# Kernel tuning notes

Measured on AMD Instinct MI355X. Metric: run time of the kernel, lower is better.

The kernel has to match this reference:

```python
import jax, jax.numpy as jnp
import numpy as np

D_MODEL = 1024
D_STATE = 16
DT_RANK = 64  # ceil(1024/16)
DT_MIN, DT_MAX = 1e-3, 1e-1


def setup_inputs() -> dict:
    key = jax.random.key(0)
    ks = jax.random.split(key, 6)
    x = jax.random.normal(ks[0], (2, 2048, D_MODEL), jnp.float32)
    A_log = jax.random.normal(ks[1], (D_MODEL, D_STATE), jnp.float32)
    D = jax.random.normal(ks[2], (D_MODEL,), jnp.float32)
    # nn.Linear default init ~ U(-1/sqrt(fan_in), 1/sqrt(fan_in)); normal*scale is fine for a baseline
    x_proj_w = jax.random.normal(ks[3], (DT_RANK + 2 * D_STATE, D_MODEL), jnp.float32) * (D_MODEL ** -0.5)
    dt_init_std = DT_RANK ** -0.5
    dt_proj_w = jax.random.uniform(ks[4], (D_MODEL, DT_RANK), jnp.float32, -dt_init_std, dt_init_std)
    dt = jnp.exp(jax.random.uniform(ks[5], (D_MODEL,), jnp.float32)
                 * (np.log(DT_MAX) - np.log(DT_MIN)) + np.log(DT_MIN))
    dt_proj_b = dt + jnp.log(-jnp.expm1(-dt))  # inverse-softplus init
    return {"x": x, "A_log": A_log, "D": D, "x_proj_w": x_proj_w,
            "dt_proj_w": dt_proj_w, "dt_proj_b": dt_proj_b}


def _s6(x, A_log, D, x_proj_w, dt_proj_w, dt_proj_b):
    A = -jnp.exp(A_log)                                    # (d, n)
    xp = jnp.einsum('bld,ed->ble', x, x_proj_w)            # (b, l, r+2n)
    d_rank = xp[..., :DT_RANK]
    Bm = xp[..., DT_RANK:DT_RANK + D_STATE]                # (b, l, n)
    Cm = xp[..., DT_RANK + D_STATE:]                       # (b, l, n)
    delta = jax.nn.softplus(jnp.einsum('blr,dr->bld', d_rank, dt_proj_w) + dt_proj_b)
    deltaA = jnp.exp(jnp.einsum('bld,dn->bldn', delta, A))          # (b, l, d, n)
    deltaB_u = jnp.einsum('bld,bln,bld->bldn', delta, Bm, x)        # (b, l, d, n)

    def step(h, inp):
        dA_t, dBu_t, C_t = inp          # (b,d,n), (b,d,n), (b,n)
        h = dA_t * h + dBu_t
        y = jnp.einsum('bdn,bn->bd', h, C_t)
        return h, y

    b, l, d = x.shape
    h0 = jnp.zeros((b, d, D_STATE), x.dtype)
    _, ys = jax.lax.scan(step, h0,
                         (deltaA.transpose(1, 0, 2, 3),
                          deltaB_u.transpose(1, 0, 2, 3),
                          Cm.transpose(1, 0, 2)))
    y = ys.transpose(1, 0, 2) + x * D                      # (b, l, d)
    return y


def reference(x, A_log, D, x_proj_w, dt_proj_w, dt_proj_b):
    return _s6(x, A_log, D, x_proj_w, dt_proj_w, dt_proj_b)
```

## Files before the change

### kernel.cpp

```cpp
#include <hip/hip_runtime.h>
#include <math.h>

#define Bb 2
#define Ll 2048
#define Dm 1024
#define Ns 16
#define Rr 64
#define Ee 96
#define XPS 8
#define BLK (Bb*Ll)
#define NTHR 256

__global__ void __launch_bounds__(NTHR)
k_xproj(const float* __restrict__ x, const float* __restrict__ xw,
        float* __restrict__ xp_part) {
    __shared__ float xs[64 * 37];
    __shared__ float wsh[96 * 37];
    int bx = blockIdx.x;
    int ks = bx & 7, mt = bx >> 3;
    int i0 = mt * 64;
    int tid = threadIdx.x;
    int tx = tid & 15, ty = tid >> 4;
    float acc[4][6];
#pragma unroll
    for (int ii = 0; ii < 4; ++ii)
#pragma unroll
        for (int jj = 0; jj < 6; ++jj) acc[ii][jj] = 0.f;

    for (int kc = 0; kc < 4; ++kc) {
        int k0 = ks * 128 + kc * 32;
        for (int t = tid; t < 512; t += NTHR) {
            int r = t >> 3, c = (t & 7) * 4;
            float4 v = *(const float4*)(x + (size_t)(i0 + r) * Dm + k0 + c);
            xs[r*37+c] = v.x; xs[r*37+c+1] = v.y; xs[r*37+c+2] = v.z; xs[r*37+c+3] = v.w;
        }
        for (int t = tid; t < 768; t += NTHR) {
            int r = t >> 3, c = (t & 7) * 4;
            float4 v = *(const float4*)(xw + (size_t)r * Dm + k0 + c);
            wsh[r*37+c] = v.x; wsh[r*37+c+1] = v.y; wsh[r*37+c+2] = v.z; wsh[r*37+c+3] = v.w;
        }
        __syncthreads();
#pragma unroll 8
        for (int k = 0; k < 32; ++k) {
            float xv[4], wv[6];
#pragma unroll
            for (int ii = 0; ii < 4; ++ii) xv[ii] = xs[(ty*4+ii)*37 + k];
#pragma unroll
            for (int jj = 0; jj < 6; ++jj) wv[jj] = wsh[(tx*6+jj)*37 + k];
#pragma unroll
            for (int ii = 0; ii < 4; ++ii)
#pragma unroll
                for (int jj = 0; jj < 6; ++jj)
                    acc[ii][jj] = fmaf(xv[ii], wv[jj], acc[ii][jj]);
        }
        __syncthreads();
    }
#pragma unroll
    for (int ii = 0; ii < 4; ++ii)
#pragma unroll
        for (int jj = 0; jj < 6; ++jj)
            xp_part[((size_t)ks * BLK + (i0 + ty*4 + ii)) * Ee + tx*6 + jj] = acc[ii][jj];
}

__global__ void __launch_bounds__(NTHR)
k_prep(const float* __restrict__ xp_part, float* __restrict__ xp) {
    int g = blockIdx.x * NTHR + threadIdx.x;
    const float4* p = (const float4*)xp_part;
    float4 s = p[g];
#pragma unroll
    for (int i = 1; i < XPS; ++i) {
        float4 v = p[(size_t)i * (BLK * Ee / 4) + g];
        s.x += v.x; s.y += v.y; s.z += v.z; s.w += v.w;
    }
    ((float4*)xp)[g] = s;
}

__global__ void __launch_bounds__(NTHR)
k_delta(const float* __restrict__ xp, const float* __restrict__ dtw,
        const float* __restrict__ dtb, float* __restrict__ delta) {
    __shared__ float xs[64 * 65];
    __shared__ float wsh[64 * 65];
    int bx = blockIdx.x;
    int nt = bx & 15, mt = bx >> 4;
    int i0 = mt * 64, j0 = nt * 64;
    int tid = threadIdx.x, tx = tid & 15, ty = tid >> 4;

    for (int t = tid; t < 1024; t += NTHR) {
        int r = t >> 4, c = (t & 15) * 4;
        float4 v = *(const float4*)(xp + (size_t)(i0 + r) * Ee + c);
        xs[r*65+c] = v.x; xs[r*65+c+1] = v.y; xs[r*65+c+2] = v.z; xs[r*65+c+3] = v.w;
        float4 w = *(const float4*)(dtw + (size_t)(j0 + r) * Rr + c);
        wsh[r*65+c] = w.x; wsh[r*65+c+1] = w.y; wsh[r*65+c+2] = w.z; wsh[r*65+c+3] = w.w;
    }
    __syncthreads();

    float acc[4][4];
#pragma unroll
    for (int ii = 0; ii < 4; ++ii)
#pragma unroll
        for (int jj = 0; jj < 4; ++jj) acc[ii][jj] = 0.f;
#pragma unroll 8
    for (int k = 0; k < 64; ++k) {
        float xv[4], wv[4];
#pragma unroll
        for (int ii = 0; ii < 4; ++ii) xv[ii] = xs[(ty*4+ii)*65 + k];
#pragma unroll
        for (int jj = 0; jj < 4; ++jj) wv[jj] = wsh[(tx*4+jj)*65 + k];
#pragma unroll
        for (int ii = 0; ii < 4; ++ii)
#pragma unroll
            for (int jj = 0; jj < 4; ++jj)
                acc[ii][jj] = fmaf(xv[ii], wv[jj], acc[ii][jj]);
    }
    int d0 = j0 + tx * 4;
    float4 bias = *(const float4*)(dtb + d0);
#pragma unroll
    for (int ii = 0; ii < 4; ++ii) {
        int bl = i0 + ty*4 + ii;
        float z0 = acc[ii][0] + bias.x, z1 = acc[ii][1] + bias.y;
        float z2 = acc[ii][2] + bias.z, z3 = acc[ii][3] + bias.w;
        float4 o;
        o.x = fmaxf(z0, 0.f) + log1pf(__expf(-fabsf(z0)));
        o.y = fmaxf(z1, 0.f) + log1pf(__expf(-fabsf(z1)));
        o.z = fmaxf(z2, 0.f) + log1pf(__expf(-fabsf(z2)));
        o.w = fmaxf(z3, 0.f) + log1pf(__expf(-fabsf(z3)));
        *(float4*)(delta + (size_t)bl * Dm + d0) = o;
    }
}

__device__ inline void load_a(const float* __restrict__ A_log, int d, float* a) {
    const float4* Ap = (const float4*)(A_log + (size_t)d * Ns);
    float4 a0 = Ap[0], a1 = Ap[1], a2 = Ap[2], a3 = Ap[3];
    float tmp[Ns] = {a0.x,a0.y,a0.z,a0.w, a1.x,a1.y,a1.z,a1.w,
                     a2.x,a2.y,a2.z,a2.w, a3.x,a3.y,a3.z,a3.w};
#pragma unroll
    for (int n = 0; n < Ns; ++n) a[n] = -__expf(tmp[n]);
}

template<int CHv>
__global__ void __launch_bounds__(NTHR)
k_scan_part(const float* __restrict__ delta, const float* __restrict__ x,
            const float* __restrict__ xp, const float* __restrict__ A_log,
            float* __restrict__ Ec, float* __restrict__ Sc) {
    constexpr int CLv = Ll / CHv;
    int bx = blockIdx.x;
    int dblk = bx & 3, chunk = (bx >> 2) & (CHv - 1), b = bx >> 2 >> __builtin_ctz(CHv);
    int tid = threadIdx.x;
    int d = dblk * 256 + tid;
    int row0 = b * Ll + chunk * CLv;

    float a[Ns], h[Ns];
    load_a(A_log, d, a);
#pragma unroll
    for (int n = 0; n < Ns; ++n) h[n] = 0.f;
    float sd = 0.f;

#pragma unroll 4
    for (int t = 0; t < CLv; ++t) {
        size_t row = (size_t)(row0 + t);
        float dl = delta[row * Dm + d];
        float xv = x[row * Dm + d];
        const float* bp = xp + row * Ee + Rr;
        float4 B0 = *(const float4*)(bp + 0),  B1 = *(const float4*)(bp + 4);
        float4 B2 = *(const float4*)(bp + 8),  B3 = *(const float4*)(bp + 12);
        float Bv[Ns] = {B0.x,B0.y,B0.z,B0.w, B1.x,B1.y,B1.z,B1.w,
                        B2.x,B2.y,B2.z,B2.w, B3.x,B3.y,B3.z,B3.w};
        float dx = dl * xv;
        sd += dl;
#pragma unroll
        for (int n = 0; n < Ns; ++n)
            h[n] = fmaf(__expf(dl * a[n]), h[n], dx * Bv[n]);
    }
    size_t base = ((size_t)b * CHv + chunk) * Dm + d;
    float4* Ep = (float4*)(Ec + base * Ns);
    Ep[0] = make_float4(h[0],  h[1],  h[2],  h[3]);
    Ep[1] = make_float4(h[4],  h[5],  h[6],  h[7]);
    Ep[2] = make_float4(h[8],  h[9],  h[10], h[11]);
    Ep[3] = make_float4(h[12], h[13], h[14], h[15]);
    Sc[base] = sd;
}

template<int CHv>
__global__ void __launch_bounds__(NTHR)
k_combine(const float* __restrict__ Ec, const float* __restrict__ Sc,
          const float* __restrict__ A_log, float* __restrict__ Hin) {
    int gid = blockIdx.x * NTHR + threadIdx.x;
    int n = gid & (Ns - 1);
    int d = (gid >> 4) & (Dm - 1);
    int b = gid >> 14;
    float a = -__expf(A_log[d * Ns + n]);
    float h = 0.f;
    for (int c = 0; c < CHv; ++c) {
        size_t base = ((size_t)b * CHv + c) * Dm + d;
        Hin[base * Ns + n] = h;
        float P = __expf(a * Sc[base]);
        h = fmaf(P, h, Ec[base * Ns + n]);
    }
}

template<int CHv>
__global__ void __launch_bounds__(NTHR)
k_scan_full(const float* __restrict__ delta, const float* __restrict__ x,
            const float* __restrict__ xp, const float* __restrict__ A_log,
            const float* __restrict__ Dp, const float* __restrict__ Hin,
            float* __restrict__ out) {
    constexpr int CLv = Ll / CHv;
    int bx = blockIdx.x;
    int dblk = bx & 3, chunk = (bx >> 2) & (CHv - 1), b = bx >> 2 >> __builtin_ctz(CHv);
    int tid = threadIdx.x;
    int d = dblk * 256 + tid;
    int row0 = b * Ll + chunk * CLv;

    float a[Ns], h[Ns];
    load_a(A_log, d, a);
    size_t base = ((size_t)b * CHv + chunk) * Dm + d;
    {
        const float4* Hp = (const float4*)(Hin + base * Ns);
        float4 h0 = Hp[0], h1 = Hp[1], h2 = Hp[2], h3 = Hp[3];
        h[0]=h0.x; h[1]=h0.y; h[2]=h0.z; h[3]=h0.w;
        h[4]=h1.x; h[5]=h1.y; h[6]=h1.z; h[7]=h1.w;
        h[8]=h2.x; h[9]=h2.y; h[10]=h2.z; h[11]=h2.w;
        h[12]=h3.x; h[13]=h3.y; h[14]=h3.z; h[15]=h3.w;
    }
    float Dval = Dp[d];

#pragma unroll 4
    for (int t = 0; t < CLv; ++t) {
        size_t row = (size_t)(row0 + t);
        float dl = delta[row * Dm + d];
        float xv = x[row * Dm + d];
        const float* bp = xp + row * Ee + Rr;
        float4 B0 = *(const float4*)(bp + 0),  B1 = *(const float4*)(bp + 4);
        float4 B2 = *(const float4*)(bp + 8),  B3 = *(const float4*)(bp + 12);
        float4 C0 = *(const float4*)(bp + 16), C1 = *(const float4*)(bp + 20);
        float4 C2 = *(const float4*)(bp + 24), C3 = *(const float4*)(bp + 28);
        float Bv[Ns] = {B0.x,B0.y,B0.z,B0.w, B1.x,B1.y,B1.z,B1.w,
                        B2.x,B2.y,B2.z,B2.w, B3.x,B3.y,B3.z,B3.w};
        float Cv[Ns] = {C0.x,C0.y,C0.z,C0.w, C1.x,C1.y,C1.z,C1.w,
                        C2.x,C2.y,C2.z,C2.w, C3.x,C3.y,C3.z,C3.w};
        float dx = dl * xv;
        float y = 0.f;
#pragma unroll
        for (int n = 0; n < Ns; ++n) {
            h[n] = fmaf(__expf(dl * a[n]), h[n], dx * Bv[n]);
            y = fmaf(h[n], Cv[n], y);
        }
        out[row * Dm + d] = fmaf(xv, Dval, y);
    }
}

extern "C" void kernel_launch(void* const* d_in, const int* in_sizes, int n_in,
                              void* d_out, int out_size, void* d_ws, size_t ws_size,
                              hipStream_t stream) {
    const float* x     = (const float*)d_in[0];
    const float* A_log = (const float*)d_in[1];
    const float* Dp    = (const float*)d_in[2];
    const float* xw    = (const float*)d_in[3];
    const float* dtw   = (const float*)d_in[4];
    const float* dtb   = (const float*)d_in[5];
    float* out = (float*)d_out;
    float* ws  = (float*)d_ws;

    float* xp      = ws;
    float* delta   = xp + 393216;
    float* S3      = delta + 4194304;
    float* xp_part = S3;

    k_xproj<<<dim3(512),  dim3(NTHR), 0, stream>>>(x, xw, xp_part);
    k_prep <<<dim3(384),  dim3(NTHR), 0, stream>>>(xp_part, xp);
    k_delta<<<dim3(1024), dim3(NTHR), 0, stream>>>(xp, dtw, dtb, delta);

    size_t need128 = (size_t)(393216 + 4194304 + 8650752) * 4;
    if (ws_size >= need128) {
        constexpr int CHv = 128;
        float* Ec  = S3;
        float* Sc  = Ec + (size_t)Bb*CHv*Dm*Ns;
        float* Hin = Sc + (size_t)Bb*CHv*Dm;
        k_scan_part<CHv><<<dim3(Bb*CHv*4), dim3(NTHR), 0, stream>>>(delta, x, xp, A_log, Ec, Sc);
        k_combine  <CHv><<<dim3(128),      dim3(NTHR), 0, stream>>>(Ec, Sc, A_log, Hin);
        k_scan_full<CHv><<<dim3(Bb*CHv*4), dim3(NTHR), 0, stream>>>(delta, x, xp, A_log, Dp, Hin, out);
    } else {
        constexpr int CHv = 64;
        float* Ec  = S3;
        float* Sc  = Ec + (size_t)Bb*CHv*Dm*Ns;
        float* Hin = Sc + (size_t)Bb*CHv*Dm;
        k_scan_part<CHv><<<dim3(Bb*CHv*4), dim3(NTHR), 0, stream>>>(delta, x, xp, A_log, Ec, Sc);
        k_combine  <CHv><<<dim3(128),      dim3(NTHR), 0, stream>>>(Ec, Sc, A_log, Hin);
        k_scan_full<CHv><<<dim3(Bb*CHv*4), dim3(NTHR), 0, stream>>>(delta, x, xp, A_log, Dp, Hin, out);
    }
}
```

Measured before the change: 165.4 us.

## Fuse split-K reduction, delta projection and chunk scan into one kernel

Merges the split-K partial-sum reduction, the dt projection with softplus, and the first-pass chunk scan into a single kernel. Delta and B values for each 64-row tile stay in shared memory and feed the local scan without a round trip through global memory. The chunk count is fixed at 64 chunks of 32 steps. The x-projection tile grows to 128 rows, with transposed shared layouts that allow vector LDS reads. Only 256 blocks run the fused kernel and each uses large shared memory, so occupancy and parallelism in the scan phase drop.

```diff
diff --git a/kernel.cpp b/kernel.cpp
--- a/kernel.cpp
+++ b/kernel.cpp
@@ -10,45 +10,51 @@
 #define XPS 8
 #define BLK (Bb*Ll)
 #define NTHR 256
+#define CH 64
+#define CL 32
 
 __global__ void __launch_bounds__(NTHR)
 k_xproj(const float* __restrict__ x, const float* __restrict__ xw,
         float* __restrict__ xp_part) {
-    __shared__ float xs[64 * 37];
-    __shared__ float wsh[96 * 37];
+    __shared__ float xsT[32 * 132];
+    __shared__ float wT [32 * 100];
     int bx = blockIdx.x;
     int ks = bx & 7, mt = bx >> 3;
-    int i0 = mt * 64;
+    int i0 = mt * 128;
     int tid = threadIdx.x;
     int tx = tid & 15, ty = tid >> 4;
-    float acc[4][6];
-#pragma unroll
-    for (int ii = 0; ii < 4; ++ii)
+
+    float acc[8][6];
+#pragma unroll
+    for (int ii = 0; ii < 8; ++ii)
 #pragma unroll
         for (int jj = 0; jj < 6; ++jj) acc[ii][jj] = 0.f;
 
     for (int kc = 0; kc < 4; ++kc) {
         int k0 = ks * 128 + kc * 32;
-        for (int t = tid; t < 512; t += NTHR) {
+        for (int t = tid; t < 1024; t += NTHR) {
             int r = t >> 3, c = (t & 7) * 4;
             float4 v = *(const float4*)(x + (size_t)(i0 + r) * Dm + k0 + c);
-            xs[r*37+c] = v.x; xs[r*37+c+1] = v.y; xs[r*37+c+2] = v.z; xs[r*37+c+3] = v.w;
+            xsT[(c+0)*132 + r] = v.x; xsT[(c+1)*132 + r] = v.y;
+            xsT[(c+2)*132 + r] = v.z; xsT[(c+3)*132 + r] = v.w;
         }
         for (int t = tid; t < 768; t += NTHR) {
             int r = t >> 3, c = (t & 7) * 4;
             float4 v = *(const float4*)(xw + (size_t)r * Dm + k0 + c);
-            wsh[r*37+c] = v.x; wsh[r*37+c+1] = v.y; wsh[r*37+c+2] = v.z; wsh[r*37+c+3] = v.w;
+            wT[(c+0)*100 + r] = v.x; wT[(c+1)*100 + r] = v.y;
+            wT[(c+2)*100 + r] = v.z; wT[(c+3)*100 + r] = v.w;
         }
         __syncthreads();
 #pragma unroll 8
         for (int k = 0; k < 32; ++k) {
-            float xv[4], wv[6];
-#pragma unroll
-            for (int ii = 0; ii < 4; ++ii) xv[ii] = xs[(ty*4+ii)*37 + k];
-#pragma unroll
-            for (int jj = 0; jj < 6; ++jj) wv[jj] = wsh[(tx*6+jj)*37 + k];
-#pragma unroll
-            for (int ii = 0; ii < 4; ++ii)
+            float xv[8], wv[6];
+            *(float4*)(xv)   = *(const float4*)(xsT + k*132 + ty*8);
+            *(float4*)(xv+4) = *(const float4*)(xsT + k*132 + ty*8 + 4);
+            *(float2*)(wv)   = *(const float2*)(wT + k*100 + tx*6);
+            *(float2*)(wv+2) = *(const float2*)(wT + k*100 + tx*6 + 2);
+            *(float2*)(wv+4) = *(const float2*)(wT + k*100 + tx*6 + 4);
+#pragma unroll
+            for (int ii = 0; ii < 8; ++ii)
 #pragma unroll
                 for (int jj = 0; jj < 6; ++jj)
                     acc[ii][jj] = fmaf(xv[ii], wv[jj], acc[ii][jj]);
@@ -56,131 +62,139 @@
         __syncthreads();
     }
 #pragma unroll
-    for (int ii = 0; ii < 4; ++ii)
+    for (int ii = 0; ii < 8; ++ii)
 #pragma unroll
         for (int jj = 0; jj < 6; ++jj)
-            xp_part[((size_t)ks * BLK + (i0 + ty*4 + ii)) * Ee + tx*6 + jj] = acc[ii][jj];
-}
-
-__global__ void __launch_bounds__(NTHR)
-k_prep(const float* __restrict__ xp_part, float* __restrict__ xp) {
-    int g = blockIdx.x * NTHR + threadIdx.x;
-    const float4* p = (const float4*)xp_part;
-    float4 s = p[g];
-#pragma unroll
-    for (int i = 1; i < XPS; ++i) {
-        float4 v = p[(size_t)i * (BLK * Ee / 4) + g];
-        s.x += v.x; s.y += v.y; s.z += v.z; s.w += v.w;
-    }
-    ((float4*)xp)[g] = s;
-}
-
-__global__ void __launch_bounds__(NTHR)
-k_delta(const float* __restrict__ xp, const float* __restrict__ dtw,
-        const float* __restrict__ dtb, float* __restrict__ delta) {
-    __shared__ float xs[64 * 65];
-    __shared__ float wsh[64 * 65];
+            xp_part[((size_t)ks * BLK + (i0 + ty*8 + ii)) * Ee + tx*6 + jj] = acc[ii][jj];
+}
+
+__global__ void __launch_bounds__(NTHR)
+k_dscan(const float* __restrict__ xp_part, const float* __restrict__ dtw,
+        const float* __restrict__ dtb, const float* __restrict__ x,
+        const float* __restrict__ A_log,
+        float* __restrict__ delta, float* __restrict__ xpBC,
+        float* __restrict__ Ec, float* __restrict__ Sc) {
+    __shared__ float xsT[64 * 68];
+    __shared__ float wdT[64 * 260];
+    __shared__ float BCs[64 * 33];
     int bx = blockIdx.x;
-    int nt = bx & 15, mt = bx >> 4;
-    int i0 = mt * 64, j0 = nt * 64;
-    int tid = threadIdx.x, tx = tid & 15, ty = tid >> 4;
+    int nt = bx & 3, mt = bx >> 2;
+    int i0 = mt * 64, j0 = nt * 256;
+    int tid = threadIdx.x;
+    int tx = tid & 15, ty = tid >> 4;
 
     for (int t = tid; t < 1024; t += NTHR) {
         int r = t >> 4, c = (t & 15) * 4;
-        float4 v = *(const float4*)(xp + (size_t)(i0 + r) * Ee + c);
-        xs[r*65+c] = v.x; xs[r*65+c+1] = v.y; xs[r*65+c+2] = v.z; xs[r*65+c+3] = v.w;
-        float4 w = *(const float4*)(dtw + (size_t)(j0 + r) * Rr + c);
-        wsh[r*65+c] = w.x; wsh[r*65+c+1] = w.y; wsh[r*65+c+2] = w.z; wsh[r*65+c+3] = w.w;
+        float4 s = make_float4(0.f, 0.f, 0.f, 0.f);
+#pragma unroll
+        for (int sI = 0; sI < XPS; ++sI) {
+            float4 v = *(const float4*)(xp_part + ((size_t)sI * BLK + i0 + r) * Ee + c);
+            s.x += v.x; s.y += v.y; s.z += v.z; s.w += v.w;
+        }
+        xsT[(c+0)*68 + r] = s.x; xsT[(c+1)*68 + r] = s.y;
+        xsT[(c+2)*68 + r] = s.z; xsT[(c+3)*68 + r] = s.w;
+    }
+    for (int t = tid; t < 512; t += NTHR) {
+        int r = t >> 3, cc = (t & 7) * 4;
+        float4 s = make_float4(0.f, 0.f, 0.f, 0.f);
+#pragma unroll
+        for (int sI = 0; sI < XPS; ++sI) {
+            float4 v = *(const float4*)(xp_part + ((size_t)sI * BLK + i0 + r) * Ee + Rr + cc);
+            s.x += v.x; s.y += v.y; s.z += v.z; s.w += v.w;
+        }
+        BCs[r*33 + cc+0] = s.x; BCs[r*33 + cc+1] = s.y;
+        BCs[r*33 + cc+2] = s.z; BCs[r*33 + cc+3] = s.w;
+        if (nt == 0) *(float4*)(xpBC + (size_t)(i0 + r) * 32 + cc) = s;
+    }
+    for (int t = tid; t < 4096; t += NTHR) {
+        int r = t >> 4, c = (t & 15) * 4;
+        float4 v = *(const float4*)(dtw + (size_t)(j0 + r) * Rr + c);
+        wdT[(c+0)*260 + r] = v.x; wdT[(c+1)*260 + r] = v.y;
+        wdT[(c+2)*260 + r] = v.z; wdT[(c+3)*260 + r] = v.w;
     }
     __syncthreads();
 
-    float acc[4][4];
+    float acc[4][16];
 #pragma unroll
     for (int ii = 0; ii < 4; ++ii)
 #pragma unroll
-        for (int jj = 0; jj < 4; ++jj) acc[ii][jj] = 0.f;
-#pragma unroll 8
+        for (int jj = 0; jj < 16; ++jj) acc[ii][jj] = 0.f;
+#pragma unroll 4
     for (int k = 0; k < 64; ++k) {
-        float xv[4], wv[4];
-#pragma unroll
-        for (int ii = 0; ii < 4; ++ii) xv[ii] = xs[(ty*4+ii)*65 + k];
-#pragma unroll
-        for (int jj = 0; jj < 4; ++jj) wv[jj] = wsh[(tx*4+jj)*65 + k];
+        float xv[4], wv[16];
+        *(float4*)xv = *(const float4*)(xsT + k*68 + ty*4);
+#pragma unroll
+        for (int g = 0; g < 4; ++g)
+            *(float4*)(wv + 4*g) = *(const float4*)(wdT + k*260 + g*64 + tx*4);
 #pragma unroll
         for (int ii = 0; ii < 4; ++ii)
 #pragma unroll
-            for (int jj = 0; jj < 4; ++jj)
+            for (int jj = 0; jj < 16; ++jj)
                 acc[ii][jj] = fmaf(xv[ii], wv[jj], acc[ii][jj]);
     }
-    int d0 = j0 + tx * 4;
-    float4 bias = *(const float4*)(dtb + d0);
-#pragma unroll
-    for (int ii = 0; ii < 4; ++ii) {
-        int bl = i0 + ty*4 + ii;
-        float z0 = acc[ii][0] + bias.x, z1 = acc[ii][1] + bias.y;
-        float z2 = acc[ii][2] + bias.z, z3 = acc[ii][3] + bias.w;
-        float4 o;
-        o.x = fmaxf(z0, 0.f) + log1pf(__expf(-fabsf(z0)));
-        o.y = fmaxf(z1, 0.f) + log1pf(__expf(-fabsf(z1)));
-        o.z = fmaxf(z2, 0.f) + log1pf(__expf(-fabsf(z2)));
-        o.w = fmaxf(z3, 0.f) + log1pf(__expf(-fabsf(z3)));
-        *(float4*)(delta + (size_t)bl * Dm + d0) = o;
-    }
-}
-
-__device__ inline void load_a(const float* __restrict__ A_log, int d, float* a) {
-    const float4* Ap = (const float4*)(A_log + (size_t)d * Ns);
-    float4 a0 = Ap[0], a1 = Ap[1], a2 = Ap[2], a3 = Ap[3];
-    float tmp[Ns] = {a0.x,a0.y,a0.z,a0.w, a1.x,a1.y,a1.z,a1.w,
-                     a2.x,a2.y,a2.z,a2.w, a3.x,a3.y,a3.z,a3.w};
-#pragma unroll
-    for (int n = 0; n < Ns; ++n) a[n] = -__expf(tmp[n]);
-}
-
-template<int CHv>
-__global__ void __launch_bounds__(NTHR)
-k_scan_part(const float* __restrict__ delta, const float* __restrict__ x,
-            const float* __restrict__ xp, const float* __restrict__ A_log,
-            float* __restrict__ Ec, float* __restrict__ Sc) {
-    constexpr int CLv = Ll / CHv;
-    int bx = blockIdx.x;
-    int dblk = bx & 3, chunk = (bx >> 2) & (CHv - 1), b = bx >> 2 >> __builtin_ctz(CHv);
-    int tid = threadIdx.x;
-    int d = dblk * 256 + tid;
-    int row0 = b * Ll + chunk * CLv;
-
-    float a[Ns], h[Ns];
-    load_a(A_log, d, a);
-#pragma unroll
-    for (int n = 0; n < Ns; ++n) h[n] = 0.f;
-    float sd = 0.f;
-
+    __syncthreads();
+
+    float* deltaT = wdT;
+#pragma unroll
+    for (int g = 0; g < 4; ++g) {
+        int dl0 = g*64 + tx*4;
+        float4 bias = *(const float4*)(dtb + j0 + dl0);
+#pragma unroll
+        for (int ii = 0; ii < 4; ++ii) {
+            int tloc = ty*4 + ii;
+            float z0 = acc[ii][g*4+0] + bias.x, z1 = acc[ii][g*4+1] + bias.y;
+            float z2 = acc[ii][g*4+2] + bias.z, z3 = acc[ii][g*4+3] + bias.w;
+            float4 o;
+            o.x = fmaxf(z0, 0.f) + log1pf(__expf(-fabsf(z0)));
+            o.y = fmaxf(z1, 0.f) + log1pf(__expf(-fabsf(z1)));
+            o.z = fmaxf(z2, 0.f) + log1pf(__expf(-fabsf(z2)));
+            o.w = fmaxf(z3, 0.f) + log1pf(__expf(-fabsf(z3)));
+            *(float4*)(deltaT + tloc*260 + dl0) = o;
+            *(float4*)(delta + (size_t)(i0 + tloc) * Dm + j0 + dl0) = o;
+        }
+    }
+    __syncthreads();
+
+    int dloc = tid, d = j0 + dloc;
+    float a[Ns];
+    {
+        const float4* Ap = (const float4*)(A_log + (size_t)d * Ns);
+        float4 a0 = Ap[0], a1 = Ap[1], a2 = Ap[2], a3 = Ap[3];
+        float tmp[Ns] = {a0.x,a0.y,a0.z,a0.w, a1.x,a1.y,a1.z,a1.w,
+                         a2.x,a2.y,a2.z,a2.w, a3.x,a3.y,a3.z,a3.w};
+#pragma unroll
+        for (int n = 0; n < Ns; ++n) a[n] = -__expf(tmp[n]);
+    }
+#pragma unroll
+    for (int ch = 0; ch < 2; ++ch) {
+        int row0 = i0 + ch * CL;
+        int b = row0 >> 11, c = (row0 & (Ll - 1)) >> 5;
+        float h[Ns];
+#pragma unroll
+        for (int n = 0; n < Ns; ++n) h[n] = 0.f;
+        float sd = 0.f;
 #pragma unroll 4
-    for (int t = 0; t < CLv; ++t) {
-        size_t row = (size_t)(row0 + t);
-        float dl = delta[row * Dm + d];
-        float xv = x[row * Dm + d];
-        const float* bp = xp + row * Ee + Rr;
-        float4 B0 = *(const float4*)(bp + 0),  B1 = *(const float4*)(bp + 4);
-        float4 B2 = *(const float4*)(bp + 8),  B3 = *(const float4*)(bp + 12);
-        float Bv[Ns] = {B0.x,B0.y,B0.z,B0.w, B1.x,B1.y,B1.z,B1.w,
-                        B2.x,B2.y,B2.z,B2.w, B3.x,B3.y,B3.z,B3.w};
-        float dx = dl * xv;
-        sd += dl;
-#pragma unroll
-        for (int n = 0; n < Ns; ++n)
-            h[n] = fmaf(__expf(dl * a[n]), h[n], dx * Bv[n]);
-    }
-    size_t base = ((size_t)b * CHv + chunk) * Dm + d;
-    float4* Ep = (float4*)(Ec + base * Ns);
-    Ep[0] = make_float4(h[0],  h[1],  h[2],  h[3]);
-    Ep[1] = make_float4(h[4],  h[5],  h[6],  h[7]);
-    Ep[2] = make_float4(h[8],  h[9],  h[10], h[11]);
-    Ep[3] = make_float4(h[12], h[13], h[14], h[15]);
-    Sc[base] = sd;
-}
-
-template<int CHv>
+        for (int t = 0; t < CL; ++t) {
+            int tloc = ch * CL + t;
+            float dl = deltaT[tloc*260 + dloc];
+            float xv = x[(size_t)(row0 + t) * Dm + d];
+            float dx = dl * xv;
+            sd += dl;
+            const float* bp = BCs + tloc*33;
+#pragma unroll
+            for (int n = 0; n < Ns; ++n)
+                h[n] = fmaf(__expf(dl * a[n]), h[n], dx * bp[n]);
+        }
+        size_t base = ((size_t)b * CH + c) * Dm + d;
+        float4* Ep = (float4*)(Ec + base * Ns);
+        Ep[0] = make_float4(h[0],  h[1],  h[2],  h[3]);
+        Ep[1] = make_float4(h[4],  h[5],  h[6],  h[7]);
+        Ep[2] = make_float4(h[8],  h[9],  h[10], h[11]);
+        Ep[3] = make_float4(h[12], h[13], h[14], h[15]);
+        Sc[base] = sd;
+    }
+}
+
 __global__ void __launch_bounds__(NTHR)
 k_combine(const float* __restrict__ Ec, const float* __restrict__ Sc,
           const float* __restrict__ A_log, float* __restrict__ Hin) {
@@ -190,30 +204,35 @@
     int b = gid >> 14;
     float a = -__expf(A_log[d * Ns + n]);
     float h = 0.f;
-    for (int c = 0; c < CHv; ++c) {
-        size_t base = ((size_t)b * CHv + c) * Dm + d;
+    for (int c = 0; c < CH; ++c) {
+        size_t base = ((size_t)b * CH + c) * Dm + d;
         Hin[base * Ns + n] = h;
         float P = __expf(a * Sc[base]);
         h = fmaf(P, h, Ec[base * Ns + n]);
     }
 }
 
-template<int CHv>
 __global__ void __launch_bounds__(NTHR)
 k_scan_full(const float* __restrict__ delta, const float* __restrict__ x,
-            const float* __restrict__ xp, const float* __restrict__ A_log,
+            const float* __restrict__ xpBC, const float* __restrict__ A_log,
             const float* __restrict__ Dp, const float* __restrict__ Hin,
             float* __restrict__ out) {
-    constexpr int CLv = Ll / CHv;
     int bx = blockIdx.x;
-    int dblk = bx & 3, chunk = (bx >> 2) & (CHv - 1), b = bx >> 2 >> __builtin_ctz(CHv);
+    int dblk = bx & 3, chunk = (bx >> 2) & (CH - 1), b = bx >> 8;
     int tid = threadIdx.x;
     int d = dblk * 256 + tid;
-    int row0 = b * Ll + chunk * CLv;
+    int row0 = b * Ll + chunk * CL;
 
     float a[Ns], h[Ns];
-    load_a(A_log, d, a);
-    size_t base = ((size_t)b * CHv + chunk) * Dm + d;
+    {
+        const float4* Ap = (const float4*)(A_log + (size_t)d * Ns);
+        float4 a0 = Ap[0], a1 = Ap[1], a2 = Ap[2], a3 = Ap[3];
+        float tmp[Ns] = {a0.x,a0.y,a0.z,a0.w, a1.x,a1.y,a1.z,a1.w,
+                         a2.x,a2.y,a2.z,a2.w, a3.x,a3.y,a3.z,a3.w};
+#pragma unroll
+        for (int n = 0; n < Ns; ++n) a[n] = -__expf(tmp[n]);
+    }
+    size_t base = ((size_t)b * CH + chunk) * Dm + d;
     {
         const float4* Hp = (const float4*)(Hin + base * Ns);
         float4 h0 = Hp[0], h1 = Hp[1], h2 = Hp[2], h3 = Hp[3];
@@ -225,11 +244,11 @@
     float Dval = Dp[d];
 
 #pragma unroll 4
-    for (int t = 0; t < CLv; ++t) {
+    for (int t = 0; t < CL; ++t) {
         size_t row = (size_t)(row0 + t);
         float dl = delta[row * Dm + d];
         float xv = x[row * Dm + d];
-        const float* bp = xp + row * Ee + Rr;
+        const float* bp = xpBC + row * 32;
         float4 B0 = *(const float4*)(bp + 0),  B1 = *(const float4*)(bp + 4);
         float4 B2 = *(const float4*)(bp + 8),  B3 = *(const float4*)(bp + 12);
         float4 C0 = *(const float4*)(bp + 16), C1 = *(const float4*)(bp + 20);
@@ -261,31 +280,16 @@
     float* out = (float*)d_out;
     float* ws  = (float*)d_ws;
 
-    float* xp      = ws;
-    float* delta   = xp + 393216;
-    float* S3      = delta + 4194304;
-    float* xp_part = S3;
-
-    k_xproj<<<dim3(512),  dim3(NTHR), 0, stream>>>(x, xw, xp_part);
-    k_prep <<<dim3(384),  dim3(NTHR), 0, stream>>>(xp_part, xp);
-    k_delta<<<dim3(1024), dim3(NTHR), 0, stream>>>(xp, dtw, dtb, delta);
-
-    size_t need128 = (size_t)(393216 + 4194304 + 8650752) * 4;
-    if (ws_size >= need128) {
-        constexpr int CHv = 128;
-        float* Ec  = S3;
-        float* Sc  = Ec + (size_t)Bb*CHv*Dm*Ns;
-        float* Hin = Sc + (size_t)Bb*CHv*Dm;
-        k_scan_part<CHv><<<dim3(Bb*CHv*4), dim3(NTHR), 0, stream>>>(delta, x, xp, A_log, Ec, Sc);
-        k_combine  <CHv><<<dim3(128),      dim3(NTHR), 0, stream>>>(Ec, Sc, A_log, Hin);
-        k_scan_full<CHv><<<dim3(Bb*CHv*4), dim3(NTHR), 0, stream>>>(delta, x, xp, A_log, Dp, Hin, out);
-    } else {
-        constexpr int CHv = 64;
-        float* Ec  = S3;
-        float* Sc  = Ec + (size_t)Bb*CHv*Dm*Ns;
-        float* Hin = Sc + (size_t)Bb*CHv*Dm;
-        k_scan_part<CHv><<<dim3(Bb*CHv*4), dim3(NTHR), 0, stream>>>(delta, x, xp, A_log, Ec, Sc);
-        k_combine  <CHv><<<dim3(128),      dim3(NTHR), 0, stream>>>(Ec, Sc, A_log, Hin);
-        k_scan_full<CHv><<<dim3(Bb*CHv*4), dim3(NTHR), 0, stream>>>(delta, x, xp, A_log, Dp, Hin, out);
-    }
-}
+    float* delta   = ws;
+    float* xpBC    = delta   + 4194304;
+    float* xp_part = xpBC    + 131072;
+    float* Ec      = xp_part + 3145728;
+    float* Sc      = Ec      + 2097152;
+    float* Hin     = Sc      + 131072;
+
+    k_xproj    <<<dim3(256), dim3(NTHR), 0, stream>>>(x, xw, xp_part);
+    k_dscan    <<<dim3(256), dim3(NTHR), 0, stream>>>(xp_part, dtw, dtb, x, A_log,
+                                                      delta, xpBC, Ec, Sc);
+    k_combine  <<<dim3(128), dim3(NTHR), 0, stream>>>(Ec, Sc, A_log, Hin);
+    k_scan_full<<<dim3(512), dim3(NTHR), 0, stream>>>(delta, x, xpBC, A_log, Dp, Hin, out);
+}
```

New measurement: 169.6 us. +2.5%, slower.

## Transpose GEMM smem tiles for vector loads and stage B/C in shared memory

Applied to the files above, without the earlier changes.

The x-projection and delta GEMMs now store their shared-memory tiles transposed (k-major with padding), so the inner loop reads operands with float4/float2 vector LDS instead of scalar strided reads. The prep kernel splits xp into a separate dt-rank buffer and a compact B/C buffer. Both scan kernels copy their chunk's B/C rows into shared memory once per block and read them from there, and they get a launch-bounds occupancy hint. The transposed tile stores may cause bank conflicts on the write side, and the occupancy hint may limit registers for the scan.

```diff
diff --git a/kernel.cpp b/kernel.cpp
--- a/kernel.cpp
+++ b/kernel.cpp
@@ -14,13 +14,14 @@
 __global__ void __launch_bounds__(NTHR)
 k_xproj(const float* __restrict__ x, const float* __restrict__ xw,
         float* __restrict__ xp_part) {
-    __shared__ float xs[64 * 37];
-    __shared__ float wsh[96 * 37];
+    __shared__ float xsT[32 * 68];
+    __shared__ float wT [32 * 100];
     int bx = blockIdx.x;
     int ks = bx & 7, mt = bx >> 3;
     int i0 = mt * 64;
     int tid = threadIdx.x;
     int tx = tid & 15, ty = tid >> 4;
+
     float acc[4][6];
 #pragma unroll
     for (int ii = 0; ii < 4; ++ii)
@@ -32,21 +33,23 @@
         for (int t = tid; t < 512; t += NTHR) {
             int r = t >> 3, c = (t & 7) * 4;
             float4 v = *(const float4*)(x + (size_t)(i0 + r) * Dm + k0 + c);
-            xs[r*37+c] = v.x; xs[r*37+c+1] = v.y; xs[r*37+c+2] = v.z; xs[r*37+c+3] = v.w;
+            xsT[(c+0)*68 + r] = v.x; xsT[(c+1)*68 + r] = v.y;
+            xsT[(c+2)*68 + r] = v.z; xsT[(c+3)*68 + r] = v.w;
         }
         for (int t = tid; t < 768; t += NTHR) {
             int r = t >> 3, c = (t & 7) * 4;
             float4 v = *(const float4*)(xw + (size_t)r * Dm + k0 + c);
-            wsh[r*37+c] = v.x; wsh[r*37+c+1] = v.y; wsh[r*37+c+2] = v.z; wsh[r*37+c+3] = v.w;
+            wT[(c+0)*100 + r] = v.x; wT[(c+1)*100 + r] = v.y;
+            wT[(c+2)*100 + r] = v.z; wT[(c+3)*100 + r] = v.w;
         }
         __syncthreads();
 #pragma unroll 8
         for (int k = 0; k < 32; ++k) {
             float xv[4], wv[6];
-#pragma unroll
-            for (int ii = 0; ii < 4; ++ii) xv[ii] = xs[(ty*4+ii)*37 + k];
-#pragma unroll
-            for (int jj = 0; jj < 6; ++jj) wv[jj] = wsh[(tx*6+jj)*37 + k];
+            *(float4*)xv     = *(const float4*)(xsT + k*68 + ty*4);
+            *(float2*)(wv)   = *(const float2*)(wT + k*100 + tx*6);
+            *(float2*)(wv+2) = *(const float2*)(wT + k*100 + tx*6 + 2);
+            *(float2*)(wv+4) = *(const float2*)(wT + k*100 + tx*6 + 4);
 #pragma unroll
             for (int ii = 0; ii < 4; ++ii)
 #pragma unroll
@@ -63,23 +66,25 @@
 }
 
 __global__ void __launch_bounds__(NTHR)
-k_prep(const float* __restrict__ xp_part, float* __restrict__ xp) {
-    int g = blockIdx.x * NTHR + threadIdx.x;
-    const float4* p = (const float4*)xp_part;
-    float4 s = p[g];
-#pragma unroll
-    for (int i = 1; i < XPS; ++i) {
-        float4 v = p[(size_t)i * (BLK * Ee / 4) + g];
+k_prep(const float* __restrict__ xp_part, float* __restrict__ xpR,
+       float* __restrict__ xpBC) {
+    int gid = blockIdx.x * NTHR + threadIdx.x;
+    int r = gid / 24, c4 = gid % 24;
+    float4 s = make_float4(0.f, 0.f, 0.f, 0.f);
+#pragma unroll
+    for (int i = 0; i < XPS; ++i) {
+        float4 v = *(const float4*)(xp_part + ((size_t)i * BLK + r) * Ee + c4 * 4);
         s.x += v.x; s.y += v.y; s.z += v.z; s.w += v.w;
     }
-    ((float4*)xp)[g] = s;
+    if (c4 < 16) *(float4*)(xpR  + (size_t)r * Rr + c4 * 4)        = s;
+    else         *(float4*)(xpBC + (size_t)r * 32 + (c4 - 16) * 4) = s;
 }
 
 __global__ void __launch_bounds__(NTHR)
-k_delta(const float* __restrict__ xp, const float* __restrict__ dtw,
+k_delta(const float* __restrict__ xpR, const float* __restrict__ dtw,
         const float* __restrict__ dtb, float* __restrict__ delta) {
-    __shared__ float xs[64 * 65];
-    __shared__ float wsh[64 * 65];
+    __shared__ float xsT[64 * 68];
+    __shared__ float wT [64 * 68];
     int bx = blockIdx.x;
     int nt = bx & 15, mt = bx >> 4;
     int i0 = mt * 64, j0 = nt * 64;
@@ -87,10 +92,12 @@
 
     for (int t = tid; t < 1024; t += NTHR) {
         int r = t >> 4, c = (t & 15) * 4;
-        float4 v = *(const float4*)(xp + (size_t)(i0 + r) * Ee + c);
-        xs[r*65+c] = v.x; xs[r*65+c+1] = v.y; xs[r*65+c+2] = v.z; xs[r*65+c+3] = v.w;
+        float4 v = *(const float4*)(xpR + (size_t)(i0 + r) * Rr + c);
+        xsT[(c+0)*68 + r] = v.x; xsT[(c+1)*68 + r] = v.y;
+        xsT[(c+2)*68 + r] = v.z; xsT[(c+3)*68 + r] = v.w;
         float4 w = *(const float4*)(dtw + (size_t)(j0 + r) * Rr + c);
-        wsh[r*65+c] = w.x; wsh[r*65+c+1] = w.y; wsh[r*65+c+2] = w.z; wsh[r*65+c+3] = w.w;
+        wT[(c+0)*68 + r] = w.x; wT[(c+1)*68 + r] = w.y;
+        wT[(c+2)*68 + r] = w.z; wT[(c+3)*68 + r] = w.w;
     }
     __syncthreads();
 
@@ -102,10 +109,8 @@
 #pragma unroll 8
     for (int k = 0; k < 64; ++k) {
         float xv[4], wv[4];
-#pragma unroll
-        for (int ii = 0; ii < 4; ++ii) xv[ii] = xs[(ty*4+ii)*65 + k];
-#pragma unroll
-        for (int jj = 0; jj < 4; ++jj) wv[jj] = wsh[(tx*4+jj)*65 + k];
+        *(float4*)xv = *(const float4*)(xsT + k*68 + ty*4);
+        *(float4*)wv = *(const float4*)(wT  + k*68 + tx*4);
 #pragma unroll
         for (int ii = 0; ii < 4; ++ii)
 #pragma unroll
@@ -138,29 +143,35 @@
 }
 
 template<int CHv>
-__global__ void __launch_bounds__(NTHR)
+__global__ void __launch_bounds__(NTHR, 4)
 k_scan_part(const float* __restrict__ delta, const float* __restrict__ x,
-            const float* __restrict__ xp, const float* __restrict__ A_log,
+            const float* __restrict__ xpBC, const float* __restrict__ A_log,
             float* __restrict__ Ec, float* __restrict__ Sc) {
     constexpr int CLv = Ll / CHv;
+    __shared__ float BCs[CLv * 32];
     int bx = blockIdx.x;
     int dblk = bx & 3, chunk = (bx >> 2) & (CHv - 1), b = bx >> 2 >> __builtin_ctz(CHv);
     int tid = threadIdx.x;
     int d = dblk * 256 + tid;
     int row0 = b * Ll + chunk * CLv;
 
+    for (int t = tid; t < CLv * 8; t += NTHR) {
+        int r = t >> 3, c = (t & 7) * 4;
+        *(float4*)(BCs + r*32 + c) = *(const float4*)(xpBC + (size_t)(row0 + r) * 32 + c);
+    }
     float a[Ns], h[Ns];
     load_a(A_log, d, a);
 #pragma unroll
     for (int n = 0; n < Ns; ++n) h[n] = 0.f;
     float sd = 0.f;
+    __syncthreads();
 
 #pragma unroll 4
     for (int t = 0; t < CLv; ++t) {
         size_t row = (size_t)(row0 + t);
         float dl = delta[row * Dm + d];
         float xv = x[row * Dm + d];
-        const float* bp = xp + row * Ee + Rr;
+        const float* bp = BCs + t*32;
         float4 B0 = *(const float4*)(bp + 0),  B1 = *(const float4*)(bp + 4);
         float4 B2 = *(const float4*)(bp + 8),  B3 = *(const float4*)(bp + 12);
         float Bv[Ns] = {B0.x,B0.y,B0.z,B0.w, B1.x,B1.y,B1.z,B1.w,
@@ -199,18 +210,23 @@
 }
 
 template<int CHv>
-__global__ void __launch_bounds__(NTHR)
+__global__ void __launch_bounds__(NTHR, 4)
 k_scan_full(const float* __restrict__ delta, const float* __restrict__ x,
-            const float* __restrict__ xp, const float* __restrict__ A_log,
+            const float* __restrict__ xpBC, const float* __restrict__ A_log,
             const float* __restrict__ Dp, const float* __restrict__ Hin,
             float* __restrict__ out) {
     constexpr int CLv = Ll / CHv;
+    __shared__ float BCs[CLv * 32];
     int bx = blockIdx.x;
     int dblk = bx & 3, chunk = (bx >> 2) & (CHv - 1), b = bx >> 2 >> __builtin_ctz(CHv);
     int tid = threadIdx.x;
     int d = dblk * 256 + tid;
     int row0 = b * Ll + chunk * CLv;
 
+    for (int t = tid; t < CLv * 8; t += NTHR) {
+        int r = t >> 3, c = (t & 7) * 4;
+        *(float4*)(BCs + r*32 + c) = *(const float4*)(xpBC + (size_t)(row0 + r) * 32 + c);
+    }
     float a[Ns], h[Ns];
     load_a(A_log, d, a);
     size_t base = ((size_t)b * CHv + chunk) * Dm + d;
@@ -223,13 +239,14 @@
         h[12]=h3.x; h[13]=h3.y; h[14]=h3.z; h[15]=h3.w;
     }
     float Dval = Dp[d];
+    __syncthreads();
 
 #pragma unroll 4
     for (int t = 0; t < CLv; ++t) {
         size_t row = (size_t)(row0 + t);
         float dl = delta[row * Dm + d];
         float xv = x[row * Dm + d];
-        const float* bp = xp + row * Ee + Rr;
+        const float* bp = BCs + t*32;
         float4 B0 = *(const float4*)(bp + 0),  B1 = *(const float4*)(bp + 4);
         float4 B2 = *(const float4*)(bp + 8),  B3 = *(const float4*)(bp + 12);
         float4 C0 = *(const float4*)(bp + 16), C1 = *(const float4*)(bp + 20);
@@ -261,31 +278,32 @@
     float* out = (float*)d_out;
     float* ws  = (float*)d_ws;
 
-    float* xp      = ws;
-    float* delta   = xp + 393216;
+    float* xpR     = ws;
+    float* xpBC    = xpR  + 262144;
+    float* delta   = xpBC + 131072;
     float* S3      = delta + 4194304;
     float* xp_part = S3;
 
     k_xproj<<<dim3(512),  dim3(NTHR), 0, stream>>>(x, xw, xp_part);
-    k_prep <<<dim3(384),  dim3(NTHR), 0, stream>>>(xp_part, xp);
-    k_delta<<<dim3(1024), dim3(NTHR), 0, stream>>>(xp, dtw, dtb, delta);
-
-    size_t need128 = (size_t)(393216 + 4194304 + 8650752) * 4;
+    k_prep <<<dim3(384),  dim3(NTHR), 0, stream>>>(xp_part, xpR, xpBC);
+    k_delta<<<dim3(1024), dim3(NTHR), 0, stream>>>(xpR, dtw, dtb, delta);
+
+    size_t need128 = (size_t)(262144 + 131072 + 4194304 + 8650752) * 4;
     if (ws_size >= need128) {
         constexpr int CHv = 128;
         float* Ec  = S3;
         float* Sc  = Ec + (size_t)Bb*CHv*Dm*Ns;
         float* Hin = Sc + (size_t)Bb*CHv*Dm;
-        k_scan_part<CHv><<<dim3(Bb*CHv*4), dim3(NTHR), 0, stream>>>(delta, x, xp, A_log, Ec, Sc);
+        k_scan_part<CHv><<<dim3(Bb*CHv*4), dim3(NTHR), 0, stream>>>(delta, x, xpBC, A_log, Ec, Sc);
         k_combine  <CHv><<<dim3(128),      dim3(NTHR), 0, stream>>>(Ec, Sc, A_log, Hin);
-        k_scan_full<CHv><<<dim3(Bb*CHv*4), dim3(NTHR), 0, stream>>>(delta, x, xp, A_log, Dp, Hin, out);
+        k_scan_full<CHv><<<dim3(Bb*CHv*4), dim3(NTHR), 0, stream>>>(delta, x, xpBC, A_log, Dp, Hin, out);
     } else {
         constexpr int CHv = 64;
         float* Ec  = S3;
         float* Sc  = Ec + (size_t)Bb*CHv*Dm*Ns;
         float* Hin = Sc + (size_t)Bb*CHv*Dm;
-        k_scan_part<CHv><<<dim3(Bb*CHv*4), dim3(NTHR), 0, stream>>>(delta, x, xp, A_log, Ec, Sc);
+        k_scan_part<CHv><<<dim3(Bb*CHv*4), dim3(NTHR), 0, stream>>>(delta, x, xpBC, A_log, Ec, Sc);
         k_combine  <CHv><<<dim3(128),      dim3(NTHR), 0, stream>>>(Ec, Sc, A_log, Hin);
-        k_scan_full<CHv><<<dim3(Bb*CHv*4), dim3(NTHR), 0, stream>>>(delta, x, xp, A_log, Dp, Hin, out);
-    }
-}
+        k_scan_full<CHv><<<dim3(Bb*CHv*4), dim3(NTHR), 0, stream>>>(delta, x, xpBC, A_log, Dp, Hin, out);
+    }
+}
```

After: 167.5 us. No clear change (+1.3%).
